# Optimization experiments

Measured on AMD Instinct MI355X. Metric: run time of the kernel, lower is better.

## Reference

```python
import jax, jax.numpy as jnp
import numpy as np

IN_DIM, OUT_DIM, NUM_KNOTS = 256, 256, 20
X_MIN, X_MAX = -5.0, 5.0
H = (X_MAX - X_MIN) / (NUM_KNOTS - 1)  # uniform knot spacing


def setup_inputs() -> dict:
    key = jax.random.key(0)
    k1, k2 = jax.random.split(key, 2)
    x = jax.random.normal(k1, (1024, IN_DIM), dtype=jnp.float32) * 2.0
    # per-(out,in)-pair cubic coefficients for each of the NUM_KNOTS-1 intervals: [a,b,c,d]
    coeffs = jax.random.normal(k2, (OUT_DIM, IN_DIM, NUM_KNOTS - 1, 4), dtype=jnp.float32) * 0.1
    bias = jnp.zeros((OUT_DIM,), dtype=jnp.float32)
    return {"x": x, "coeffs": coeffs, "bias": bias}


def reference(x, coeffs, bias):
    # x: [B, I]; coeffs: [J, I, K, 4]; bias: [J]
    B, I = x.shape
    K = coeffs.shape[2]
    # locate knot interval (clamped -> linear-cubic extrapolation at edges)
    idx = jnp.clip(jnp.floor((x - X_MIN) / H).astype(jnp.int32), 0, K - 1)  # [B, I]
    t = x - (X_MIN + idx.astype(x.dtype) * H)                               # [B, I]
    # gather per-pair interval coefficients: [J, B, I, 4]
    i_arr = jnp.broadcast_to(jnp.arange(I)[None, :], idx.shape)
    c = coeffs[:, i_arr, idx]
    a, b, c2, d = c[..., 0], c[..., 1], c[..., 2], c[..., 3]
    # Horner evaluation; t broadcasts [B,I] -> [J,B,I]
    y = ((d * t + c2) * t + b) * t + a
    # sum over input dims, add bias: [B, J]
    return y.sum(axis=-1).T + bias[None, :]
```

## Files before the change

kernel.cpp:

```cpp
#include <hip/hip_runtime.h>

#define IN_DIM   256
#define OUT_DIM  256
#define NKNOT    19
#define NCOL     (IN_DIM * NKNOT)
#define CPQ      1216
#define PLANE_U4 (CPQ * 32)
#define SLICE_U4 (PLANE_U4 * 2)
#define X_MIN_C  (-5.0f)
#define H_C      (10.0f / 19.0f)
#define INV_H_C  (19.0f / 10.0f)

__device__ __forceinline__ unsigned int pk_bf16(float x, float y) {
    unsigned int ux = __float_as_uint(x); ux += 0x7FFFu + ((ux >> 16) & 1u);
    unsigned int uy = __float_as_uint(y); uy += 0x7FFFu + ((uy >> 16) & 1u);
    return (ux >> 16) | (uy & 0xFFFF0000u);
}
__device__ __forceinline__ float lo16(unsigned int u) { return __uint_as_float(u << 16); }
__device__ __forceinline__ float hi16(unsigned int u) { return __uint_as_float(u & 0xFFFF0000u); }

__global__ __launch_bounds__(256) void transpose_pack(
        const float4* __restrict__ src, uint4* __restrict__ dst) {
    __shared__ float4 tile[64][65];
    const int c0 = (blockIdx.x % 76) * 64;
    const int r0 = (blockIdx.x / 76) * 64;
    const int tx = threadIdx.x & 63;
    const int ty = threadIdx.x >> 6;

    #pragma unroll
    for (int jj = 0; jj < 16; ++jj) {
        const int r = ty * 16 + jj;
        tile[tx][r] = src[(size_t)(r0 + r) * NCOL + (size_t)(c0 + tx)];
    }
    __syncthreads();

    const int quarter = c0 / CPQ;
    const int clbase  = c0 - quarter * CPQ;
    const int o_half  = r0 >> 7;
    const int og_base = (r0 & 127) >> 2;
    uint4* base = dst + (size_t)(quarter * 2 + o_half) * SLICE_U4;

    #pragma unroll
    for (int jj = 0; jj < 4; ++jj) {
        const int p  = jj * 256 + threadIdx.x;
        const int cl = p >> 4;
        const int og = p & 15;
        const float4 v0 = tile[cl][og * 4 + 0];
        const float4 v1 = tile[cl][og * 4 + 1];
        const float4 v2 = tile[cl][og * 4 + 2];
        const float4 v3 = tile[cl][og * 4 + 3];
        uint4 ab, cd;
        ab.x = pk_bf16(v0.x, v1.x); ab.y = pk_bf16(v2.x, v3.x);
        ab.z = pk_bf16(v0.y, v1.y); ab.w = pk_bf16(v2.y, v3.y);
        cd.x = pk_bf16(v0.z, v1.z); cd.y = pk_bf16(v2.z, v3.z);
        cd.z = pk_bf16(v0.w, v1.w); cd.w = pk_bf16(v2.w, v3.w);
        const size_t e = (size_t)(clbase + cl) * 32 + (og_base + og);
        base[e]            = ab;
        base[PLANE_U4 + e] = cd;
    }
}

__global__ __launch_bounds__(256, 4) void kan_partial(
        const float* __restrict__ x,
        const uint4* __restrict__ Ct,
        float4*      __restrict__ part,
        int n4q) {
    __shared__ int2 s_tk[8 * 64];

    const int s       = blockIdx.x & 7;
    const int o_half  = s & 1;
    const int quarter = s >> 1;
    const int bgrp    = blockIdx.x >> 3;
    const int tid     = threadIdx.x;

    {
        const int col = tid & 63;
        const int row = tid >> 6;
        #pragma unroll
        for (int bs = row; bs < 8; bs += 4) {
            const float xv = x[(bgrp * 8 + bs) * IN_DIM + quarter * 64 + col];
            const float f  = (xv - X_MIN_C) * INV_H_C;
            int idx = (int)floorf(f);
            idx = idx < 0 ? 0 : (idx > NKNOT - 1 ? NKNOT - 1 : idx);
            s_tk[bs * 64 + col] =
                make_int2(idx * 32, __float_as_int(xv - (X_MIN_C + (float)idx * H_C)));
        }
    }
    __syncthreads();

    const int og = tid & 31;
    const int bs = tid >> 5;
    const uint4* baseAB = Ct + (size_t)s * SLICE_U4 + og;
    const uint4* baseCD = baseAB + PLANE_U4;
    const int2* tkp = s_tk + bs * 64;

    float y0 = 0.f, y1 = 0.f, y2 = 0.f, y3 = 0.f;

    #pragma unroll 4
    for (int ii = 0; ii < 64; ++ii) {
        const int2 tk = tkp[ii];
        const int  e  = ii * 608 + tk.x;
        const uint4 AB = baseAB[e];
        const uint4 CD = baseCD[e];
        const float t  = __int_as_float(tk.y);
        const float a_0 = lo16(AB.x), a_1 = hi16(AB.x), a_2 = lo16(AB.y), a_3 = hi16(AB.y);
        const float b_0 = lo16(AB.z), b_1 = hi16(AB.z), b_2 = lo16(AB.w), b_3 = hi16(AB.w);
        const float c_0 = lo16(CD.x), c_1 = hi16(CD.x), c_2 = lo16(CD.y), c_3 = hi16(CD.y);
        const float d_0 = lo16(CD.z), d_1 = hi16(CD.z), d_2 = lo16(CD.w), d_3 = hi16(CD.w);
        y0 += ((d_0 * t + c_0) * t + b_0) * t + a_0;
        y1 += ((d_1 * t + c_1) * t + b_1) * t + a_1;
        y2 += ((d_2 * t + c_2) * t + b_2) * t + a_2;
        y3 += ((d_3 * t + c_3) * t + b_3) * t + a_3;
    }

    const int b = bgrp * 8 + bs;
    part[(size_t)quarter * n4q + (size_t)b * 64 + (o_half * 32 + og)] =
        make_float4(y0, y1, y2, y3);
}

__global__ __launch_bounds__(256) void kan_reduce(
        const float4* __restrict__ part,
        const float4* __restrict__ bias4,
        float4*       __restrict__ out,
        int n4) {
    const int n = blockIdx.x * 256 + threadIdx.x;
    if (n < n4) {
        const float4 p0 = part[n];
        const float4 p1 = part[n4 + n];
        const float4 p2 = part[2 * n4 + n];
        const float4 p3 = part[3 * n4 + n];
        const float4 bv = bias4[n & 63];
        float4 r;
        r.x = (p0.x + p1.x) + (p2.x + p3.x) + bv.x;
        r.y = (p0.y + p1.y) + (p2.y + p3.y) + bv.y;
        r.z = (p0.z + p1.z) + (p2.z + p3.z) + bv.z;
        r.w = (p0.w + p1.w) + (p2.w + p3.w) + bv.w;
        out[n] = r;
    }
}

extern "C" void kernel_launch(void* const* d_in, const int* in_sizes, int n_in,
                              void* d_out, int out_size, void* d_ws, size_t ws_size,
                              hipStream_t stream) {
    const float* x      = (const float*)d_in[0];
    const float* coeffs = (const float*)d_in[1];
    const float* bias   = (const float*)d_in[2];
    float*       out    = (float*)d_out;

    const int B = in_sizes[0] / IN_DIM;
    uint4* Ct   = (uint4*)d_ws;
    float* part = (float*)((char*)d_ws + (16u << 20));

    transpose_pack<<<304, 256, 0, stream>>>((const float4*)coeffs, Ct);

    const int n4 = B * OUT_DIM / 4;
    kan_partial<<<B, 256, 0, stream>>>(x, Ct, (float4*)part, n4);
    kan_reduce<<<(n4 + 255) / 256, 256, 0, stream>>>(
        (const float4*)part, (const float4*)bias, (float4*)out, n4);
}
```

Baseline: 100.5 us.

## Map one wavefront per batch row and broadcast interval data via readlane

Reorganizes the coefficient layout so each lane covers four outputs across all 256, and assigns one wavefront per batch row per input quarter. Interval index and offset are precomputed by a separate kernel into global memory and broadcast within the wave with readlane, removing LDS staging and the block barrier. This makes the gather address wave-uniform and the loads fully contiguous, at the cost of an extra kernel launch and a global round trip for the precomputed values.

```diff
diff --git a/kernel.cpp b/kernel.cpp
--- a/kernel.cpp
+++ b/kernel.cpp
@@ -5,7 +5,7 @@
 #define NKNOT    19
 #define NCOL     (IN_DIM * NKNOT)
 #define CPQ      1216
-#define PLANE_U4 (CPQ * 32)
+#define PLANE_U4 (CPQ * 64)
 #define SLICE_U4 (PLANE_U4 * 2)
 #define X_MIN_C  (-5.0f)
 #define H_C      (10.0f / 19.0f)
@@ -34,11 +34,10 @@
     }
     __syncthreads();
 
-    const int quarter = c0 / CPQ;
-    const int clbase  = c0 - quarter * CPQ;
-    const int o_half  = r0 >> 7;
-    const int og_base = (r0 & 127) >> 2;
-    uint4* base = dst + (size_t)(quarter * 2 + o_half) * SLICE_U4;
+    const int quarter  = c0 / CPQ;
+    const int clbase   = c0 - quarter * CPQ;
+    const int og_base  = r0 >> 2;
+    uint4* base = dst + (size_t)quarter * SLICE_U4;
 
     #pragma unroll
     for (int jj = 0; jj < 4; ++jj) {
@@ -54,55 +53,47 @@
         ab.z = pk_bf16(v0.y, v1.y); ab.w = pk_bf16(v2.y, v3.y);
         cd.x = pk_bf16(v0.z, v1.z); cd.y = pk_bf16(v2.z, v3.z);
         cd.z = pk_bf16(v0.w, v1.w); cd.w = pk_bf16(v2.w, v3.w);
-        const size_t e = (size_t)(clbase + cl) * 32 + (og_base + og);
+        const size_t e = (size_t)(clbase + cl) * 64 + (og_base + og);
         base[e]            = ab;
         base[PLANE_U4 + e] = cd;
     }
 }
 
+__global__ __launch_bounds__(256) void make_tk(
+        const float* __restrict__ x, int2* __restrict__ tkg, int Btot) {
+    const int n = blockIdx.x * 256 + threadIdx.x;
+    if (n >= Btot * IN_DIM) return;
+    const float xv = x[n];
+    int idx = (int)floorf((xv - X_MIN_C) * INV_H_C);
+    idx = idx < 0 ? 0 : (idx > NKNOT - 1 ? NKNOT - 1 : idx);
+    tkg[n] = make_int2(idx, __float_as_int(xv - (X_MIN_C + (float)idx * H_C)));
+}
+
 __global__ __launch_bounds__(256, 4) void kan_partial(
-        const float* __restrict__ x,
+        const int2*  __restrict__ tkg,
         const uint4* __restrict__ Ct,
         float4*      __restrict__ part,
-        int n4q) {
-    __shared__ int2 s_tk[8 * 64];
+        int Btot) {
+    const int q    = blockIdx.x & 3;
+    const int bgrp = blockIdx.x >> 2;
+    const int w    = threadIdx.x >> 6;
+    const int lane = threadIdx.x & 63;
+    const int b    = bgrp * 4 + w;
 
-    const int s       = blockIdx.x & 7;
-    const int o_half  = s & 1;
-    const int quarter = s >> 1;
-    const int bgrp    = blockIdx.x >> 3;
-    const int tid     = threadIdx.x;
+    const int2 tkv = tkg[b * IN_DIM + q * 64 + lane];
 
-    {
-        const int col = tid & 63;
-        const int row = tid >> 6;
-        #pragma unroll
-        for (int bs = row; bs < 8; bs += 4) {
-            const float xv = x[(bgrp * 8 + bs) * IN_DIM + quarter * 64 + col];
-            const float f  = (xv - X_MIN_C) * INV_H_C;
-            int idx = (int)floorf(f);
-            idx = idx < 0 ? 0 : (idx > NKNOT - 1 ? NKNOT - 1 : idx);
-            s_tk[bs * 64 + col] =
-                make_int2(idx * 32, __float_as_int(xv - (X_MIN_C + (float)idx * H_C)));
-        }
-    }
-    __syncthreads();
-
-    const int og = tid & 31;
-    const int bs = tid >> 5;
-    const uint4* baseAB = Ct + (size_t)s * SLICE_U4 + og;
-    const uint4* baseCD = baseAB + PLANE_U4;
-    const int2* tkp = s_tk + bs * 64;
+    const char* baseAB = (const char*)(Ct + (size_t)q * SLICE_U4) + lane * 16;
 
     float y0 = 0.f, y1 = 0.f, y2 = 0.f, y3 = 0.f;
 
     #pragma unroll 4
     for (int ii = 0; ii < 64; ++ii) {
-        const int2 tk = tkp[ii];
-        const int  e  = ii * 608 + tk.x;
-        const uint4 AB = baseAB[e];
-        const uint4 CD = baseCD[e];
-        const float t  = __int_as_float(tk.y);
+        const int   k = __builtin_amdgcn_readlane(tkv.x, ii);
+        const float t = __uint_as_float(
+            (unsigned int)__builtin_amdgcn_readlane(tkv.y, ii));
+        const size_t off = (size_t)(ii * NKNOT + k) * 1024;
+        const uint4 AB = *(const uint4*)(baseAB + off);
+        const uint4 CD = *(const uint4*)(baseAB + (size_t)PLANE_U4 * 16 + off);
         const float a_0 = lo16(AB.x), a_1 = hi16(AB.x), a_2 = lo16(AB.y), a_3 = hi16(AB.y);
         const float b_0 = lo16(AB.z), b_1 = hi16(AB.z), b_2 = lo16(AB.w), b_3 = hi16(AB.w);
         const float c_0 = lo16(CD.x), c_1 = hi16(CD.x), c_2 = lo16(CD.y), c_3 = hi16(CD.y);
@@ -113,9 +104,7 @@
         y3 += ((d_3 * t + c_3) * t + b_3) * t + a_3;
     }
 
-    const int b = bgrp * 8 + bs;
-    part[(size_t)quarter * n4q + (size_t)b * 64 + (o_half * 32 + og)] =
-        make_float4(y0, y1, y2, y3);
+    part[((size_t)q * Btot + b) * 64 + lane] = make_float4(y0, y1, y2, y3);
 }
 
 __global__ __launch_bounds__(256) void kan_reduce(
@@ -149,12 +138,14 @@
 
     const int B = in_sizes[0] / IN_DIM;
     uint4* Ct   = (uint4*)d_ws;
+    int2*  tkg  = (int2*)((char*)d_ws + (12u << 20));
     float* part = (float*)((char*)d_ws + (16u << 20));
 
     transpose_pack<<<304, 256, 0, stream>>>((const float4*)coeffs, Ct);
+    make_tk<<<(B * IN_DIM + 255) / 256, 256, 0, stream>>>(x, tkg, B);
+    kan_partial<<<B, 256, 0, stream>>>(tkg, Ct, (float4*)part, B);
 
     const int n4 = B * OUT_DIM / 4;
-    kan_partial<<<B, 256, 0, stream>>>(x, Ct, (float4*)part, n4);
     kan_reduce<<<(n4 + 255) / 256, 256, 0, stream>>>(
         (const float4*)part, (const float4*)bias, (float4*)out, n4);
 }
```

New measurement: 99.30 us. About the same (-1.2%).
